# Performance work log

Hardware: AMD Instinct MI355X
Metric: run time of the kernel (lower is better)

The kernel has to match this reference:

```python
import jax, jax.numpy as jnp
import numpy as np

B, S, D_IN, D_OUT, H = 4, 2048, 768, 768, 12
DH = D_OUT // H


def setup_inputs() -> dict:
    key = jax.random.key(0)
    ks = jax.random.split(key, 6)
    x = jax.random.normal(ks[0], (B, S, D_IN), dtype=jnp.float32)
    # causal mask: True above the diagonal means "masked out" (filled with -inf)
    mask = jnp.triu(jnp.ones((S, S), dtype=bool), k=1)
    sc = 1.0 / np.sqrt(D_IN)
    Wq = jax.random.normal(ks[1], (D_IN, D_OUT), dtype=jnp.float32) * sc
    Wk = jax.random.normal(ks[2], (D_IN, D_OUT), dtype=jnp.float32) * sc
    Wv = jax.random.normal(ks[3], (D_IN, D_OUT), dtype=jnp.float32) * sc
    Wo = jax.random.normal(ks[4], (D_OUT, D_OUT), dtype=jnp.float32) * (1.0 / np.sqrt(D_OUT))
    bo = jnp.zeros((D_OUT,), dtype=jnp.float32)
    return {"input_tensor": x, "mask": mask, "Wq": Wq, "Wk": Wk, "Wv": Wv, "Wo": Wo, "bo": bo}


def reference(input_tensor, mask, Wq, Wk, Wv, Wo, bo):
    b, n, _ = input_tensor.shape
    # projections -> [b, h, n, dh]
    q = (input_tensor @ Wq).reshape(b, n, H, DH).transpose(0, 2, 1, 3)
    k = (input_tensor @ Wk).reshape(b, n, H, DH).transpose(0, 2, 1, 3)
    v = (input_tensor @ Wv).reshape(b, n, H, DH).transpose(0, 2, 1, 3)
    # scores [b, h, n, n]
    scores = jnp.einsum('bhqd,bhkd->bhqk', q, k)
    scores = jnp.where(mask[:n, :n], -jnp.inf, scores)
    attn = jax.nn.softmax(scores / np.sqrt(DH), axis=-1)
    ctx = jnp.einsum('bhqk,bhkd->bhqd', attn, v)
    ctx = ctx.transpose(0, 2, 1, 3).reshape(b, n, D_OUT)
    return ctx @ Wo + bo
```

## Files before the change

kernel.cpp:

```cpp
#include <hip/hip_runtime.h>
#include <hip/hip_bf16.h>
#include <math.h>

typedef __attribute__((ext_vector_type(4))) float f32x4;
typedef __attribute__((ext_vector_type(8))) short s16x8;
typedef __attribute__((ext_vector_type(8))) unsigned short u16x8;

#define B_ 4
#define S_ 2048
#define DIN 768
#define DOUT 768
#define H_ 12
#define DH_ 64
#define M_ (B_*S_)

__device__ __forceinline__ unsigned short f2bf(float f) {
  union { float f; unsigned u; } v; v.f = f;
  unsigned r = v.u + 0x7fffu + ((v.u >> 16) & 1u);
  return (unsigned short)(r >> 16);
}

#if __has_builtin(__builtin_amdgcn_exp2f)
#define EXP2(x) __builtin_amdgcn_exp2f(x)
#else
#define EXP2(x) exp2f(x)
#endif


__global__ __launch_bounds__(256) void prep(
    const float* __restrict__ X, unsigned short* __restrict__ Xb,
    const float* __restrict__ W0, const float* __restrict__ W1,
    const float* __restrict__ W2, const float* __restrict__ W3,
    unsigned short* __restrict__ Wt)
{
  __shared__ float t[32][33];
  const int bid = blockIdx.x;
  if (bid < 3072) {
    size_t i = ((size_t)bid * 256 + threadIdx.x) * 8;
    float4 a = *(const float4*)&X[i];
    float4 b = *(const float4*)&X[i + 4];
    u16x8 v;
    v[0] = f2bf(a.x); v[1] = f2bf(a.y); v[2] = f2bf(a.z); v[3] = f2bf(a.w);
    v[4] = f2bf(b.x); v[5] = f2bf(b.y); v[6] = f2bf(b.z); v[7] = f2bf(b.w);
    *(u16x8*)&Xb[i] = v;
  } else {
    const int t4 = bid - 3072;
    const int z = t4 / 576, rem = t4 - z * 576;
    const int ky = rem / 24, nx = rem - ky * 24;
    const float* W = z == 0 ? W0 : z == 1 ? W1 : z == 2 ? W2 : W3;
    unsigned short* Out = Wt + (size_t)z * DOUT * DIN;
    const int n0 = nx * 32, k0 = ky * 32;
    const int tx = threadIdx.x & 31, ty = threadIdx.x >> 5;
#pragma unroll
    for (int i = 0; i < 32; i += 8)
      t[ty + i][tx] = W[(size_t)(k0 + ty + i) * DOUT + n0 + tx];
    __syncthreads();
#pragma unroll
    for (int i = 0; i < 32; i += 8)
      Out[(size_t)(n0 + ty + i) * DIN + k0 + tx] = f2bf(t[tx][ty + i]);
  }
}


#define BKC 64
#define TILE_E (128 * BKC)

__device__ __forceinline__ void stage_tile(
    const unsigned short* __restrict__ g, int row0, int k0,
    unsigned short* lds, int tid)
{
#pragma unroll
  for (int it = 0; it < 4; ++it) {
    int s = it * 256 + tid;
    int row = s >> 3, sc = s & 7;
    int gc = sc ^ (row & 7);
    const unsigned short* gsrc = g + (size_t)(row0 + row) * 768 + k0 + gc * 8;
    unsigned short* dst = lds + (size_t)(it * 256 + (tid & ~63)) * 8;
    __builtin_amdgcn_global_load_lds(
        (const __attribute__((address_space(1))) void*)gsrc,
        (__attribute__((address_space(3))) void*)dst, 16, 0, 0);
  }
}

__device__ __forceinline__ void gemm_core(
    const unsigned short* __restrict__ A, const unsigned short* __restrict__ Bt,
    int m0, int n0, unsigned short* As, unsigned short* Bs,
    f32x4 acc[4][4], int tid)
{
  const int lane = tid & 63;
  const int col_l = lane & 15, quad = lane >> 4;
  const int w = tid >> 6;
  const int wm = (w & 1) * 64, wn = (w >> 1) * 64;

  stage_tile(A, m0, 0, As, tid);
  stage_tile(Bt, n0, 0, Bs, tid);

#pragma unroll 2
  for (int k0 = 0; k0 < 768; k0 += BKC) {
    const int cur = (k0 >> 6) & 1;
    const unsigned short* Asb = As + cur * TILE_E;
    const unsigned short* Bsb = Bs + cur * TILE_E;
    if (k0 + BKC < 768) {
      stage_tile(A, m0, k0 + BKC, As + (cur ^ 1) * TILE_E, tid);
      stage_tile(Bt, n0, k0 + BKC, Bs + (cur ^ 1) * TILE_E, tid);
      asm volatile("s_waitcnt vmcnt(8)" ::: "memory");
    } else {
      asm volatile("s_waitcnt vmcnt(0)" ::: "memory");
    }
    __builtin_amdgcn_s_barrier();

#pragma unroll
    for (int kk = 0; kk < 2; ++kk) {
      s16x8 af[4], bf[4];
#pragma unroll
      for (int t = 0; t < 4; ++t) {
        int ar = wm + t * 16 + col_l;
        af[t] = *(const s16x8*)&Asb[ar * BKC + (((kk << 2) + quad) ^ (ar & 7)) * 8];
        int br = wn + t * 16 + col_l;
        bf[t] = *(const s16x8*)&Bsb[br * BKC + (((kk << 2) + quad) ^ (br & 7)) * 8];
      }
#pragma unroll
      for (int mt = 0; mt < 4; ++mt)
#pragma unroll
        for (int nt = 0; nt < 4; ++nt)
          acc[mt][nt] = __builtin_amdgcn_mfma_f32_16x16x32_bf16(
              af[mt], bf[nt], acc[mt][nt], 0, 0, 0);
    }

    __builtin_amdgcn_s_barrier();
  }
}

__global__ __launch_bounds__(256) void proj_mfma(
    const unsigned short* __restrict__ Xb, const unsigned short* __restrict__ Wt,
    unsigned short* __restrict__ Qo, unsigned short* __restrict__ Ko,
    unsigned short* __restrict__ Vo)
{
  __shared__ unsigned short As[2 * TILE_E];
  __shared__ unsigned short Bs[2 * TILE_E];
  const int tid = threadIdx.x;

  const int orig = (blockIdx.z * 64 + blockIdx.y) * 6 + blockIdx.x;
  const int id = (orig & 7) * 144 + (orig >> 3);
  const int z = id / 384;
  const int r = id - z * 384;
  const int my = r / 6, nx = r - my * 6;
  const int m0 = my * 128, n0 = nx * 128;

  const unsigned short* Bw = Wt + (size_t)z * DOUT * DIN;
  unsigned short* Out = z == 0 ? Qo : z == 1 ? Ko : Vo;
  const float scale = z == 0 ? 0.125f * 1.44269504f : 1.0f;

  f32x4 acc[4][4] = {};
  gemm_core(Xb, Bw, m0, n0, As, Bs, acc, tid);

  const int lane = tid & 63, w = tid >> 6;
  const int col_l = lane & 15, quad = lane >> 4;
  const int wm = (w & 1) * 64, wn = (w >> 1) * 64;
  if (z == 2) {
    const int mblk = m0 + wm;
    const int b = mblk >> 11, sblk = mblk & (S_ - 1);
#pragma unroll
    for (int mt = 0; mt < 4; ++mt) {
      const int slot = (mt >> 1) * 32 + quad * 8 + (mt & 1) * 4;
#pragma unroll
      for (int nt = 0; nt < 4; ++nt) {
        int n = n0 + wn + nt * 16 + col_l;
        int h = n >> 6, d = n & 63;
        ushort4 v;
        v.x = f2bf(acc[mt][nt][0]); v.y = f2bf(acc[mt][nt][1]);
        v.z = f2bf(acc[mt][nt][2]); v.w = f2bf(acc[mt][nt][3]);
        *(ushort4*)&Out[((size_t)(b * H_ + h) * DH_ + d) * S_ + sblk + slot] = v;
      }
    }
  } else {
#pragma unroll
    for (int mt = 0; mt < 4; ++mt)
#pragma unroll
      for (int nt = 0; nt < 4; ++nt) {
        int n = n0 + wn + nt * 16 + col_l;
        int h = n >> 6, d = n & 63;
#pragma unroll
        for (int r2 = 0; r2 < 4; ++r2) {
          int m = m0 + wm + mt * 16 + quad * 4 + r2;
          int b = m >> 11, s = m & (S_ - 1);
          Out[((size_t)(b * H_ + h) * S_ + s) * DH_ + d] = f2bf(acc[mt][nt][r2] * scale);
        }
      }
  }
}

__global__ __launch_bounds__(256) void out_mfma(
    const unsigned short* __restrict__ Cb, const unsigned short* __restrict__ Wt,
    const float* __restrict__ bo, float* __restrict__ Out)
{
  __shared__ unsigned short As[2 * TILE_E];
  __shared__ unsigned short Bs[2 * TILE_E];
  const int tid = threadIdx.x;

  const int orig = blockIdx.y * 6 + blockIdx.x;
  const int id = (orig & 7) * 48 + (orig >> 3);
  const int my = id / 6, nx = id - my * 6;
  const int m0 = my * 128, n0 = nx * 128;

  f32x4 acc[4][4] = {};
  gemm_core(Cb, Wt, m0, n0, As, Bs, acc, tid);

  const int lane = tid & 63, w = tid >> 6;
  const int col_l = lane & 15, quad = lane >> 4;
  const int wm = (w & 1) * 64, wn = (w >> 1) * 64;
#pragma unroll
  for (int mt = 0; mt < 4; ++mt)
#pragma unroll
    for (int nt = 0; nt < 4; ++nt) {
      int n = n0 + wn + nt * 16 + col_l;
      float bias = bo[n];
#pragma unroll
      for (int r = 0; r < 4; ++r) {
        int m = m0 + wm + mt * 16 + quad * 4 + r;
        Out[(size_t)m * DOUT + n] = acc[mt][nt][r] + bias;
      }
    }
}


union PK { uint2 u2[2]; s16x8 v; };

#define MFMA_BF16 __builtin_amdgcn_mfma_f32_16x16x32_bf16

__device__ __forceinline__ void exppack(const f32x4 sc[4], PK& p0, PK& p1) {
#pragma unroll
  for (int nc = 0; nc < 4; ++nc) {
    float e0 = EXP2(sc[nc][0] - 17.3123405f);
    float e1 = EXP2(sc[nc][1] - 17.3123405f);
    float e2 = EXP2(sc[nc][2] - 17.3123405f);
    float e3 = EXP2(sc[nc][3] - 17.3123405f);
    union { __hip_bfloat162 v; unsigned u; } lo, hi;
    lo.v = __float22bfloat162_rn(make_float2(e0, e1));
    hi.v = __float22bfloat162_rn(make_float2(e2, e3));
    uint2 pw; pw.x = lo.u; pw.y = hi.u;
    if (nc < 2) p0.u2[nc] = pw; else p1.u2[nc - 2] = pw;
  }
}

__global__ __launch_bounds__(256, 3) void attn_mfma(
    const unsigned short* __restrict__ Q, const unsigned short* __restrict__ K,
    const unsigned short* __restrict__ Vt, unsigned short* __restrict__ CTX)
{
  __shared__ unsigned short Ks[2][64 * 64];
  __shared__ unsigned short Vs[2][64 * 64];

  const int tid = threadIdx.x;
  const int lane = tid & 63;
  const int w = tid >> 6;
  const int col_l = lane & 15;
  const int quad = lane >> 4;

  const int orig = (blockIdx.z * 12 + blockIdx.y) * 16 + blockIdx.x;
  const int id = (orig & 7) * 96 + (orig >> 3);
  const int p = id & 15;
  const int bh = id >> 4;
  const int h = bh % 12, b = bh / 12;

  const int q0A = p << 6, q0B = (31 - p) << 6;
  const int ntiles = 32 - p;
  const size_t bhs = (size_t)(b * H_ + h);
  const unsigned short* Qg = Q + bhs * S_ * DH_;
  const unsigned short* Kg = K + bhs * S_ * DH_;
  const unsigned short* Vg = Vt + bhs * DH_ * S_;

  const int qwA = q0A + (w << 4), qwB = q0B + (w << 4);
  s16x8 aqA0 = *(const s16x8*)&Qg[(size_t)(qwA + col_l) * DH_ + quad * 8];
  s16x8 aqA1 = *(const s16x8*)&Qg[(size_t)(qwA + col_l) * DH_ + 32 + quad * 8];
  s16x8 aqB0 = *(const s16x8*)&Qg[(size_t)(qwB + col_l) * DH_ + quad * 8];
  s16x8 aqB1 = *(const s16x8*)&Qg[(size_t)(qwB + col_l) * DH_ + 32 + quad * 8];

  const int krow = lane;
  const int kc0 = (w ^ (krow & 7)) * 8;
  const int kc1 = ((w + 4) ^ (krow & 7)) * 8;
  const int vrow = tid >> 3;
  const int vslot = tid & 7;
  const int vc = (vslot ^ (vrow & 7)) * 8;

  s16x8 kp0 = *(const s16x8*)&Kg[(size_t)krow * DH_ + w * 8];
  s16x8 kp1 = *(const s16x8*)&Kg[(size_t)krow * DH_ + (w + 4) * 8];
  s16x8 vp0 = *(const s16x8*)&Vg[(size_t)vrow * S_ + vslot * 8];
  s16x8 vp1 = *(const s16x8*)&Vg[(size_t)(vrow + 32) * S_ + vslot * 8];

  f32x4 oA[4] = {}, oB[4] = {}, lA = {}, lB = {};
  s16x8 bones;
#pragma unroll
  for (int i = 0; i < 8; ++i) bones[i] = (short)0x3F80;

  const int qrel = (w << 4) + col_l;
  const int r7 = col_l & 7;

  for (int t = 0; t < ntiles; ++t) {
    unsigned short* KsB = &Ks[t & 1][0];
    unsigned short* VsB = &Vs[t & 1][0];
    *(s16x8*)&KsB[krow * 64 + kc0] = kp0;
    *(s16x8*)&KsB[krow * 64 + kc1] = kp1;
    *(s16x8*)&VsB[vrow * 64 + vc] = vp0;
    *(s16x8*)&VsB[(vrow + 32) * 64 + vc] = vp1;
    __syncthreads();
    {
      const int jn = (t + 1 < ntiles ? t + 1 : t) << 6;
      kp0 = *(const s16x8*)&Kg[(size_t)(jn + krow) * DH_ + w * 8];
      kp1 = *(const s16x8*)&Kg[(size_t)(jn + krow) * DH_ + (w + 4) * 8];
      vp0 = *(const s16x8*)&Vg[(size_t)vrow * S_ + jn + vslot * 8];
      vp1 = *(const s16x8*)&Vg[(size_t)(vrow + 32) * S_ + jn + vslot * 8];
    }
    const bool doA = (t <= p);

    f32x4 scA[4], scB[4];
    __builtin_amdgcn_s_setprio(1);
#pragma unroll
    for (int nc = 0; nc < 4; ++nc) {
      const int kr = nc * 16 + col_l;
      s16x8 k0 = *(const s16x8*)&KsB[kr * 64 + ((quad ^ r7) * 8)];
      s16x8 k1 = *(const s16x8*)&KsB[kr * 64 + (((quad + 4) ^ r7) * 8)];
      f32x4 a = {};
      a = MFMA_BF16(k0, aqB0, a, 0, 0, 0);
      a = MFMA_BF16(k1, aqB1, a, 0, 0, 0);
      scB[nc] = a;
      if (doA) {
        f32x4 c = {};
        c = MFMA_BF16(k0, aqA0, c, 0, 0, 0);
        c = MFMA_BF16(k1, aqA1, c, 0, 0, 0);
        scA[nc] = c;
      }
    }
    __builtin_amdgcn_s_setprio(0);
    if (t == p) {
#pragma unroll
      for (int nc = 0; nc < 4; ++nc)
#pragma unroll
        for (int r = 0; r < 4; ++r)
          if (nc * 16 + quad * 4 + r > qrel) scA[nc][r] = -INFINITY;
    }
    if (t == ntiles - 1) {
#pragma unroll
      for (int nc = 0; nc < 4; ++nc)
#pragma unroll
        for (int r = 0; r < 4; ++r)
          if (nc * 16 + quad * 4 + r > qrel) scB[nc][r] = -INFINITY;
    }

    PK pA0, pA1, pB0, pB1;
    if (doA) exppack(scA, pA0, pA1);
    exppack(scB, pB0, pB1);

    __builtin_amdgcn_s_setprio(1);
#pragma unroll
    for (int dc = 0; dc < 4; ++dc) {
      const int vr = dc * 16 + col_l;
      s16x8 b0 = *(const s16x8*)&VsB[vr * 64 + ((quad ^ r7) * 8)];
      s16x8 b1 = *(const s16x8*)&VsB[vr * 64 + (((quad + 4) ^ r7) * 8)];
      oB[dc] = MFMA_BF16(pB0.v, b0, oB[dc], 0, 0, 0);
      oB[dc] = MFMA_BF16(pB1.v, b1, oB[dc], 0, 0, 0);
      if (doA) {
        oA[dc] = MFMA_BF16(pA0.v, b0, oA[dc], 0, 0, 0);
        oA[dc] = MFMA_BF16(pA1.v, b1, oA[dc], 0, 0, 0);
      }
    }
    lB = MFMA_BF16(pB0.v, bones, lB, 0, 0, 0);
    lB = MFMA_BF16(pB1.v, bones, lB, 0, 0, 0);
    if (doA) {
      lA = MFMA_BF16(pA0.v, bones, lA, 0, 0, 0);
      lA = MFMA_BF16(pA1.v, bones, lA, 0, 0, 0);
    }
    __builtin_amdgcn_s_setprio(0);
  }

  float liA[4], liB[4];
#pragma unroll
  for (int r = 0; r < 4; ++r) {
    liA[r] = 1.0f / lA[r];
    liB[r] = 1.0f / lB[r];
  }
#pragma unroll
  for (int dc = 0; dc < 4; ++dc)
#pragma unroll
    for (int r = 0; r < 4; ++r) {
      CTX[((size_t)(b * S_ + qwA + quad * 4 + r)) * DOUT + h * DH_ + dc * 16 + col_l]
          = f2bf(oA[dc][r] * liA[r]);
      CTX[((size_t)(b * S_ + qwB + quad * 4 + r)) * DOUT + h * DH_ + dc * 16 + col_l]
          = f2bf(oB[dc][r] * liB[r]);
    }
}


extern "C" void kernel_launch(void* const* d_in, const int* in_sizes, int n_in,
                              void* d_out, int out_size, void* d_ws, size_t ws_size,
                              hipStream_t stream) {
  const float* X  = (const float*)d_in[0];
  const float* Wq = (const float*)d_in[2];
  const float* Wk = (const float*)d_in[3];
  const float* Wv = (const float*)d_in[4];
  const float* Wo = (const float*)d_in[5];
  const float* bo = (const float*)d_in[6];
  float* out = (float*)d_out;

  unsigned short* Xb = (unsigned short*)d_ws;
  unsigned short* Wt = Xb + (size_t)M_ * DIN;
  unsigned short* Qb = Wt + (size_t)4 * DOUT * DIN;
  unsigned short* Kb = Qb + (size_t)M_ * DOUT;
  unsigned short* Vb = Kb + (size_t)M_ * DOUT;
  unsigned short* Cb = Vb + (size_t)M_ * DOUT;

  prep<<<dim3(3072 + 2304), 256, 0, stream>>>(X, Xb, Wq, Wk, Wv, Wo, Wt);
  proj_mfma<<<dim3(DOUT / 128, M_ / 128, 3), 256, 0, stream>>>(Xb, Wt, Qb, Kb, Vb);
  attn_mfma<<<dim3(16, H_, B_), 256, 0, stream>>>(Qb, Kb, Vb, Cb);
  out_mfma<<<dim3(DOUT / 128, M_ / 128), 256, 0, stream>>>(
      Cb, Wt + (size_t)3 * DOUT * DIN, bo, out);
}
```

Baseline: 196.6 us.

## Load K fragments directly from global into registers, bypassing LDS

K tiles are no longer staged through shared memory. Each wave now loads its MFMA K operands straight from global memory into registers and prefetches the next tile after the QK MFMAs. This removes the LDS writes, the LDS reads and half the shared-memory footprint. The cost is that every wave redundantly loads the full K tile (four times the global/L2 traffic for K) and holds 8 extra vector registers of prefetch state, which may hurt occupancy at 3 blocks per SM.

```diff
diff --git a/kernel.cpp b/kernel.cpp
--- a/kernel.cpp
+++ b/kernel.cpp
@@ -247,7 +247,6 @@
     const unsigned short* __restrict__ Q, const unsigned short* __restrict__ K,
     const unsigned short* __restrict__ Vt, unsigned short* __restrict__ CTX)
 {
-  __shared__ unsigned short Ks[2][64 * 64];
   __shared__ unsigned short Vs[2][64 * 64];
 
   const int tid = threadIdx.x;
@@ -275,15 +274,18 @@
   s16x8 aqB0 = *(const s16x8*)&Qg[(size_t)(qwB + col_l) * DH_ + quad * 8];
   s16x8 aqB1 = *(const s16x8*)&Qg[(size_t)(qwB + col_l) * DH_ + 32 + quad * 8];
 
-  const int krow = lane;
-  const int kc0 = (w ^ (krow & 7)) * 8;
-  const int kc1 = ((w + 4) ^ (krow & 7)) * 8;
+  const int koff = col_l * DH_ + quad * 8;
   const int vrow = tid >> 3;
   const int vslot = tid & 7;
   const int vc = (vslot ^ (vrow & 7)) * 8;
 
-  s16x8 kp0 = *(const s16x8*)&Kg[(size_t)krow * DH_ + w * 8];
-  s16x8 kp1 = *(const s16x8*)&Kg[(size_t)krow * DH_ + (w + 4) * 8];
+  s16x8 nk0[4], nk1[4];
+#pragma unroll
+  for (int nc = 0; nc < 4; ++nc) {
+    const unsigned short* kr = &Kg[(size_t)(nc * 16) * DH_ + koff];
+    nk0[nc] = *(const s16x8*)kr;
+    nk1[nc] = *(const s16x8*)(kr + 32);
+  }
   s16x8 vp0 = *(const s16x8*)&Vg[(size_t)vrow * S_ + vslot * 8];
   s16x8 vp1 = *(const s16x8*)&Vg[(size_t)(vrow + 32) * S_ + vslot * 8];
 
@@ -296,41 +298,45 @@
   const int r7 = col_l & 7;
 
   for (int t = 0; t < ntiles; ++t) {
-    unsigned short* KsB = &Ks[t & 1][0];
     unsigned short* VsB = &Vs[t & 1][0];
-    *(s16x8*)&KsB[krow * 64 + kc0] = kp0;
-    *(s16x8*)&KsB[krow * 64 + kc1] = kp1;
     *(s16x8*)&VsB[vrow * 64 + vc] = vp0;
     *(s16x8*)&VsB[(vrow + 32) * 64 + vc] = vp1;
     __syncthreads();
-    {
-      const int jn = (t + 1 < ntiles ? t + 1 : t) << 6;
-      kp0 = *(const s16x8*)&Kg[(size_t)(jn + krow) * DH_ + w * 8];
-      kp1 = *(const s16x8*)&Kg[(size_t)(jn + krow) * DH_ + (w + 4) * 8];
-      vp0 = *(const s16x8*)&Vg[(size_t)vrow * S_ + jn + vslot * 8];
-      vp1 = *(const s16x8*)&Vg[(size_t)(vrow + 32) * S_ + jn + vslot * 8];
-    }
+
+    s16x8 ck0[4], ck1[4];
+#pragma unroll
+    for (int nc = 0; nc < 4; ++nc) { ck0[nc] = nk0[nc]; ck1[nc] = nk1[nc]; }
+
+    const int jn = (t + 1 < ntiles ? t + 1 : t) << 6;
+    vp0 = *(const s16x8*)&Vg[(size_t)vrow * S_ + jn + vslot * 8];
+    vp1 = *(const s16x8*)&Vg[(size_t)(vrow + 32) * S_ + jn + vslot * 8];
+
     const bool doA = (t <= p);
 
     f32x4 scA[4], scB[4];
     __builtin_amdgcn_s_setprio(1);
 #pragma unroll
     for (int nc = 0; nc < 4; ++nc) {
-      const int kr = nc * 16 + col_l;
-      s16x8 k0 = *(const s16x8*)&KsB[kr * 64 + ((quad ^ r7) * 8)];
-      s16x8 k1 = *(const s16x8*)&KsB[kr * 64 + (((quad + 4) ^ r7) * 8)];
       f32x4 a = {};
-      a = MFMA_BF16(k0, aqB0, a, 0, 0, 0);
-      a = MFMA_BF16(k1, aqB1, a, 0, 0, 0);
+      a = MFMA_BF16(ck0[nc], aqB0, a, 0, 0, 0);
+      a = MFMA_BF16(ck1[nc], aqB1, a, 0, 0, 0);
       scB[nc] = a;
       if (doA) {
         f32x4 c = {};
-        c = MFMA_BF16(k0, aqA0, c, 0, 0, 0);
-        c = MFMA_BF16(k1, aqA1, c, 0, 0, 0);
+        c = MFMA_BF16(ck0[nc], aqA0, c, 0, 0, 0);
+        c = MFMA_BF16(ck1[nc], aqA1, c, 0, 0, 0);
         scA[nc] = c;
       }
     }
     __builtin_amdgcn_s_setprio(0);
+
+#pragma unroll
+    for (int nc = 0; nc < 4; ++nc) {
+      const unsigned short* kr = &Kg[(size_t)(jn + nc * 16) * DH_ + koff];
+      nk0[nc] = *(const s16x8*)kr;
+      nk1[nc] = *(const s16x8*)(kr + 32);
+    }
+
     if (t == p) {
 #pragma unroll
       for (int nc = 0; nc < 4; ++nc)
```

After: 250.0 us. 27.2% more time.

## Stage K/V tiles with direct global-to-LDS loads and vmcnt-based double buffering

Applied to the files above, without the earlier changes.

Replaces the register-staged K/V prefetch (global load into VGPRs, then ds_write) with global_load_lds instructions that write straight into the alternate LDS buffer, with an XOR swizzle applied to the source addresses. Synchronisation becomes explicit s_waitcnt vmcnt plus s_barrier, and a second barrier is added at the end of each iteration to guard buffer reuse. This is meant to remove the VGPR round-trip and the LDS write instructions, freeing registers and issue slots. In exchange there is an extra barrier per tile, and correctness depends on the hand-written vmcnt counts and the swizzled layout matching what the reads expect.

```diff
diff --git a/kernel.cpp b/kernel.cpp
--- a/kernel.cpp
+++ b/kernel.cpp
@@ -243,6 +243,32 @@
   }
 }
 
+__device__ __forceinline__ void stage_kv(
+    const unsigned short* __restrict__ Kg, const unsigned short* __restrict__ Vg,
+    int jn, unsigned short* KsB, unsigned short* VsB, int tid)
+{
+#pragma unroll
+  for (int it = 0; it < 2; ++it) {
+    int s = it * 256 + tid;
+    int row = s >> 3;
+    int gc = ((s & 7) ^ (row & 7)) * 8;
+    unsigned short* dst = KsB + (size_t)(it * 256 + (tid & ~63)) * 8;
+    __builtin_amdgcn_global_load_lds(
+        (const __attribute__((address_space(1))) void*)(Kg + (size_t)(jn + row) * DH_ + gc),
+        (__attribute__((address_space(3))) void*)dst, 16, 0, 0);
+  }
+#pragma unroll
+  for (int it = 0; it < 2; ++it) {
+    int s = it * 256 + tid;
+    int row = s >> 3;
+    int gc = ((s & 7) ^ (row & 7)) * 8;
+    unsigned short* dst = VsB + (size_t)(it * 256 + (tid & ~63)) * 8;
+    __builtin_amdgcn_global_load_lds(
+        (const __attribute__((address_space(1))) void*)(Vg + (size_t)row * S_ + jn + gc),
+        (__attribute__((address_space(3))) void*)dst, 16, 0, 0);
+  }
+}
+
 __global__ __launch_bounds__(256, 3) void attn_mfma(
     const unsigned short* __restrict__ Q, const unsigned short* __restrict__ K,
     const unsigned short* __restrict__ Vt, unsigned short* __restrict__ CTX)
@@ -275,17 +301,7 @@
   s16x8 aqB0 = *(const s16x8*)&Qg[(size_t)(qwB + col_l) * DH_ + quad * 8];
   s16x8 aqB1 = *(const s16x8*)&Qg[(size_t)(qwB + col_l) * DH_ + 32 + quad * 8];
 
-  const int krow = lane;
-  const int kc0 = (w ^ (krow & 7)) * 8;
-  const int kc1 = ((w + 4) ^ (krow & 7)) * 8;
-  const int vrow = tid >> 3;
-  const int vslot = tid & 7;
-  const int vc = (vslot ^ (vrow & 7)) * 8;
-
-  s16x8 kp0 = *(const s16x8*)&Kg[(size_t)krow * DH_ + w * 8];
-  s16x8 kp1 = *(const s16x8*)&Kg[(size_t)krow * DH_ + (w + 4) * 8];
-  s16x8 vp0 = *(const s16x8*)&Vg[(size_t)vrow * S_ + vslot * 8];
-  s16x8 vp1 = *(const s16x8*)&Vg[(size_t)(vrow + 32) * S_ + vslot * 8];
+  stage_kv(Kg, Vg, 0, &Ks[0][0], &Vs[0][0], tid);
 
   f32x4 oA[4] = {}, oB[4] = {}, lA = {}, lB = {};
   s16x8 bones;
@@ -296,20 +312,16 @@
   const int r7 = col_l & 7;
 
   for (int t = 0; t < ntiles; ++t) {
-    unsigned short* KsB = &Ks[t & 1][0];
-    unsigned short* VsB = &Vs[t & 1][0];
-    *(s16x8*)&KsB[krow * 64 + kc0] = kp0;
-    *(s16x8*)&KsB[krow * 64 + kc1] = kp1;
-    *(s16x8*)&VsB[vrow * 64 + vc] = vp0;
-    *(s16x8*)&VsB[(vrow + 32) * 64 + vc] = vp1;
-    __syncthreads();
-    {
-      const int jn = (t + 1 < ntiles ? t + 1 : t) << 6;
-      kp0 = *(const s16x8*)&Kg[(size_t)(jn + krow) * DH_ + w * 8];
-      kp1 = *(const s16x8*)&Kg[(size_t)(jn + krow) * DH_ + (w + 4) * 8];
-      vp0 = *(const s16x8*)&Vg[(size_t)vrow * S_ + jn + vslot * 8];
-      vp1 = *(const s16x8*)&Vg[(size_t)(vrow + 32) * S_ + jn + vslot * 8];
-    }
+    if (t + 1 < ntiles) {
+      stage_kv(Kg, Vg, (t + 1) << 6, &Ks[(t + 1) & 1][0], &Vs[(t + 1) & 1][0], tid);
+      asm volatile("s_waitcnt vmcnt(4)" ::: "memory");
+    } else {
+      asm volatile("s_waitcnt vmcnt(0)" ::: "memory");
+    }
+    __builtin_amdgcn_s_barrier();
+
+    const unsigned short* KsB = &Ks[t & 1][0];
+    const unsigned short* VsB = &Vs[t & 1][0];
     const bool doA = (t <= p);
 
     f32x4 scA[4], scB[4];
@@ -370,6 +382,8 @@
       lA = MFMA_BF16(pA1.v, bones, lA, 0, 0, 0);
     }
     __builtin_amdgcn_s_setprio(0);
+
+    __builtin_amdgcn_s_barrier();
   }
 
   float liA[4], liB[4];
```

New measurement: 196.6 us. No clear change (+0.0%).
